# Kernel tuning notes

Measured on AMD Instinct MI355X. Metric: run time of the kernel, lower is better.

## Reference

```python
import jax, jax.numpy as jnp
import numpy as np

NUM_HEADS = 16
HEAD_DIM = 64  # hidden_size // num_heads


def _logsparse_allowed(seq_len):
    # allowed[i, j] True if key j is attended by query i:
    # j == i, j == i-1, or j == i - 2^k (k >= 1); combined with causal (j <= i).
    i = jnp.arange(seq_len)[:, None]
    j = jnp.arange(seq_len)[None, :]
    diff = i - j
    pow2 = (diff > 0) & ((diff & (diff - 1)) == 0)  # covers diff==1 and diff==2^k
    return (diff == 0) | pow2  # implies diff >= 0, so causal is subsumed


def setup_inputs() -> dict:
    key = jax.random.key(0)
    ks = jax.random.split(key, 7)
    B, S, H = 4, 2048, 1024
    return {
        "hidden_states": jax.random.normal(ks[0], (B, S, H), dtype=jnp.float32),
        "attention_mask": jnp.zeros((B, 1, 1, S), dtype=jnp.float32),
        "Wq": jax.random.normal(ks[1], (H, H), dtype=jnp.float32) * 0.02,
        "bq": jnp.zeros((H,), dtype=jnp.float32),
        "Wk": jax.random.normal(ks[2], (H, H), dtype=jnp.float32) * 0.02,
        "bk": jnp.zeros((H,), dtype=jnp.float32),
        "Wv": jax.random.normal(ks[3], (H, H), dtype=jnp.float32) * 0.02,
        "bv": jnp.zeros((H,), dtype=jnp.float32),
    }


def _split_heads(x):
    B, S, _ = x.shape
    return x.reshape(B, S, NUM_HEADS, HEAD_DIM).transpose(0, 2, 1, 3)  # b h t d


def reference(hidden_states, attention_mask, Wq, bq, Wk, bk, Wv, bv):
    B, S, H = hidden_states.shape
    q = _split_heads(hidden_states @ Wq.T + bq)
    k = _split_heads(hidden_states @ Wk.T + bk)
    v = _split_heads(hidden_states @ Wv.T + bv)

    scores = jnp.einsum("bhqd,bhkd->bhqk", q, k) * (HEAD_DIM ** -0.5)
    allowed = _logsparse_allowed(S)  # [S, S] bool
    scores = jnp.where(allowed[None, None], scores, -jnp.inf)
    scores = scores + attention_mask  # [B,1,1,S] additive mask
    probs = jax.nn.softmax(scores, axis=-1)
    out = jnp.einsum("bhqk,bhkd->bhqd", probs, v)
    return out.transpose(0, 2, 1, 3).reshape(B, S, H)
```

## Files before the change

### kernel.cpp

```cpp
#include <hip/hip_runtime.h>
#include <hip/hip_bf16.h>

#define S_LEN   2048
#define NHEADS  16
#define HDIM    64
#define HID     1024
#define BATCH   4
#define M_ROWS  (BATCH * S_LEN)

#define BM 128
#define BN 128
#define BK 32

typedef __attribute__((ext_vector_type(8))) short short8;
typedef __attribute__((ext_vector_type(4))) float floatx4;

__device__ __forceinline__ unsigned short f2bf_rne(float x) {
  union { float f; unsigned u; } v; v.f = x;
  unsigned r = v.u + 0x7fffu + ((v.u >> 16) & 1u);
  return (unsigned short)(r >> 16);
}

__device__ __forceinline__ float bf2f(unsigned short u) {
  union { unsigned u; float f; } c; c.u = ((unsigned)u) << 16;
  return c.f;
}

__device__ __forceinline__ void glds16(const unsigned short* g, unsigned short* l) {
  __builtin_amdgcn_global_load_lds(
      (const __attribute__((address_space(1))) unsigned int*)g,
      (__attribute__((address_space(3))) unsigned int*)l, 16, 0, 0);
}

#define HS4 (M_ROWS * HID / 4)
#define W4  (HID * HID / 4)
__global__ __launch_bounds__(256) void cast_all(
    const float* __restrict__ hs, const float* __restrict__ Wq,
    const float* __restrict__ Wk, const float* __restrict__ Wv,
    unsigned short* __restrict__ hsb, unsigned short* __restrict__ wqb,
    unsigned short* __restrict__ wkb, unsigned short* __restrict__ wvb) {
  int idx = blockIdx.x * 256 + threadIdx.x;
  const float* in;
  unsigned short* out;
  int off;
  if (idx < HS4) {
    in = hs; out = hsb; off = idx;
  } else {
    int r = idx - HS4;
    int seg = r >> 18;
    off = r & (W4 - 1);
    in  = (seg == 0) ? Wq  : (seg == 1) ? Wk  : Wv;
    out = (seg == 0) ? wqb : (seg == 1) ? wkb : wvb;
  }
  float4 v = ((const float4*)in)[off];
  ushort4 o;
  o.x = f2bf_rne(v.x);
  o.y = f2bf_rne(v.y);
  o.z = f2bf_rne(v.z);
  o.w = f2bf_rne(v.w);
  ((ushort4*)out)[off] = o;
}

__global__ __launch_bounds__(256) void qkv_gemm(
    const unsigned short* __restrict__ A,
    const unsigned short* __restrict__ W0, const unsigned short* __restrict__ W1,
    const unsigned short* __restrict__ W2,
    const float* __restrict__ b0, const float* __restrict__ b1,
    const float* __restrict__ b2,
    unsigned short* __restrict__ O0, unsigned short* __restrict__ O1,
    unsigned short* __restrict__ O2) {
  const int K = HID;
  const int N = HID;
  const int z = blockIdx.z;
  const unsigned short* __restrict__ W = (z == 0) ? W0 : (z == 1) ? W1 : W2;
  const float* __restrict__ bias = (z == 0) ? b0 : (z == 1) ? b1 : b2;
  unsigned short* __restrict__ O = (z == 0) ? O0 : (z == 1) ? O1 : O2;

  __shared__ __align__(16) unsigned short As[BM * BK];
  __shared__ __align__(16) unsigned short Bs[BN * BK];

  const int tid = threadIdx.x;
  const int w = tid >> 6;
  const int lane = tid & 63;
  const int m0 = blockIdx.x * BM;
  const int n0 = blockIdx.y * BN;

  const int c0 = w * 2, c1 = w * 2 + 1;
  const int scol = (lane & 3) * 8;
  const int r0 = c0 * 16 + (lane >> 2);
  const int r1 = c1 * 16 + (lane >> 2);

  const unsigned short* gA0 = A + (size_t)(m0 + r0) * K + scol;
  const unsigned short* gA1 = A + (size_t)(m0 + r1) * K + scol;
  const unsigned short* gB0 = W + (size_t)(n0 + r0) * K + scol;
  const unsigned short* gB1 = W + (size_t)(n0 + r1) * K + scol;
  unsigned short* lA0 = As + c0 * 512;
  unsigned short* lA1 = As + c1 * 512;
  unsigned short* lB0 = Bs + c0 * 512;
  unsigned short* lB1 = Bs + c1 * 512;

  const int lrow = lane & 15;
  const int qd = lane >> 4;
  const int arow = (w & 1) * 64 + lrow;
  const int brow = (w >> 1) * 64 + lrow;

  floatx4 acc[4][4] = {};

  for (int k0 = 0; k0 < K; k0 += BK) {
    glds16(gA0 + k0, lA0);
    glds16(gA1 + k0, lA1);
    glds16(gB0 + k0, lB0);
    glds16(gB1 + k0, lB1);
    __syncthreads();

    short8 af[4], bf[4];
    #pragma unroll
    for (int im = 0; im < 4; ++im)
      af[im] = *(const short8*)(As + (arow + im * 16) * BK + qd * 8);
    #pragma unroll
    for (int in = 0; in < 4; ++in)
      bf[in] = *(const short8*)(Bs + (brow + in * 16) * BK + qd * 8);

    #pragma unroll
    for (int im = 0; im < 4; ++im)
      #pragma unroll
      for (int in = 0; in < 4; ++in)
        acc[im][in] = __builtin_amdgcn_mfma_f32_16x16x32_bf16(af[im], bf[in], acc[im][in], 0, 0, 0);
    __syncthreads();
  }

  #pragma unroll
  for (int im = 0; im < 4; ++im) {
    #pragma unroll
    for (int in = 0; in < 4; ++in) {
      const int col = n0 + (w >> 1) * 64 + in * 16 + lrow;
      const float bb = bias[col];
      #pragma unroll
      for (int r = 0; r < 4; ++r) {
        const int row = m0 + (w & 1) * 64 + im * 16 + (qd << 2) + r;
        O[(size_t)row * N + col] = f2bf_rne(acc[im][in][r] + bb);
      }
    }
  }
}

__global__ __launch_bounds__(256) void logsparse_attn(
    const unsigned short* __restrict__ Q, const unsigned short* __restrict__ K,
    const unsigned short* __restrict__ V, const float* __restrict__ mask,
    float* __restrict__ out) {
  const int tid = threadIdx.x;
  const int l = tid & 7;
  const int qglob = blockIdx.x * 32 + (tid >> 3);

  const int i = qglob & (S_LEN - 1);
  const int h = (qglob >> 11) & (NHEADS - 1);
  const int b = qglob >> 15;

  const size_t base = (size_t)b * S_LEN * HID + h * HDIM + l * 8;

  float qf[8];
  {
    short8 q8 = *(const short8*)(Q + base + (size_t)i * HID);
    #pragma unroll
    for (int e = 0; e < 8; ++e) qf[e] = bf2f((unsigned short)q8[e]);
  }

  int js[12];
  js[0] = i;
  int nj = 1;
  for (int dlt = 1; dlt <= i; dlt <<= 1) js[nj++] = i - dlt;

  float s[12];
  #pragma unroll
  for (int t = 0; t < 12; ++t) {
    if (t < nj) {
      const int j = js[t];
      short8 k8 = *(const short8*)(K + base + (size_t)j * HID);
      float p = 0.f;
      #pragma unroll
      for (int e = 0; e < 8; ++e) p += qf[e] * bf2f((unsigned short)k8[e]);
      p += __shfl_xor(p, 1, 64);
      p += __shfl_xor(p, 2, 64);
      p += __shfl_xor(p, 4, 64);
      s[t] = p * 0.125f + mask[b * S_LEN + j];
    } else {
      s[t] = -1e30f;
    }
  }

  float mx = s[0];
  #pragma unroll
  for (int t = 1; t < 12; ++t) mx = fmaxf(mx, s[t]);
  float lsum = 0.f;
  #pragma unroll
  for (int t = 0; t < 12; ++t) { s[t] = __expf(s[t] - mx); lsum += s[t]; }
  const float inv = 1.f / lsum;

  float o[8] = {};
  #pragma unroll
  for (int t = 0; t < 12; ++t) {
    if (t < nj) {
      short8 v8 = *(const short8*)(V + base + (size_t)js[t] * HID);
      #pragma unroll
      for (int e = 0; e < 8; ++e) o[e] += s[t] * bf2f((unsigned short)v8[e]);
    }
  }

  float* op = out + base + (size_t)i * HID;
  float4 o0 = {o[0] * inv, o[1] * inv, o[2] * inv, o[3] * inv};
  float4 o1 = {o[4] * inv, o[5] * inv, o[6] * inv, o[7] * inv};
  *(float4*)(op) = o0;
  *(float4*)(op + 4) = o1;
}

extern "C" void kernel_launch(void* const* d_in, const int* in_sizes, int n_in,
                              void* d_out, int out_size, void* d_ws, size_t ws_size,
                              hipStream_t stream) {
  const float* hs   = (const float*)d_in[0];
  const float* mask = (const float*)d_in[1];
  const float* Wq   = (const float*)d_in[2];
  const float* bq   = (const float*)d_in[3];
  const float* Wk   = (const float*)d_in[4];
  const float* bk   = (const float*)d_in[5];
  const float* Wv   = (const float*)d_in[6];
  const float* bv   = (const float*)d_in[7];
  float* out = (float*)d_out;

  unsigned short* hsb = (unsigned short*)d_ws;
  unsigned short* wqb = hsb + (size_t)M_ROWS * HID;
  unsigned short* wkb = wqb + (size_t)HID * HID;
  unsigned short* wvb = wkb + (size_t)HID * HID;
  unsigned short* Qb = wvb + (size_t)HID * HID;
  unsigned short* Kb = Qb + (size_t)M_ROWS * HID;
  unsigned short* Vb = Kb + (size_t)M_ROWS * HID;

  {
    int quads = HS4 + 3 * W4;
    cast_all<<<quads / 256, 256, 0, stream>>>(hs, Wq, Wk, Wv, hsb, wqb, wkb, wvb);
  }

  {
    dim3 grid(M_ROWS / BM, HID / BN, 3);
    qkv_gemm<<<grid, 256, 0, stream>>>(hsb, wqb, wkb, wvb, bq, bk, bv, Qb, Kb, Vb);
  }

  {
    int blocks = (BATCH * NHEADS * S_LEN) / 32;
    logsparse_attn<<<blocks, 256, 0, stream>>>(Qb, Kb, Vb, mask, out);
  }
}
```

Baseline: 195.2 us.

## Double GEMM K-tile with XOR-swizzled LDS and batch attention gathers upfront

The QKV GEMM K-tile grows from 32 to 64, so each barrier pair covers two MFMA k-steps. The LDS layout gets an XOR swizzle on 16-byte chunks to avoid bank conflicts on fragment reads. The attention kernel now pads the index list and issues all 12 K, V and mask loads before any compute, exposing memory-level parallelism instead of serialising loads inside predicated loops. This costs more registers and some redundant loads for short rows.

```diff
diff --git a/kernel.cpp b/kernel.cpp
--- a/kernel.cpp
+++ b/kernel.cpp
@@ -10,7 +10,7 @@
 
 #define BM 128
 #define BN 128
-#define BK 32
+#define BK 64
 
 typedef __attribute__((ext_vector_type(8))) short short8;
 typedef __attribute__((ext_vector_type(4))) float floatx4;
@@ -85,47 +85,55 @@
   const int m0 = blockIdx.x * BM;
   const int n0 = blockIdx.y * BN;
 
-  const int c0 = w * 2, c1 = w * 2 + 1;
-  const int scol = (lane & 3) * 8;
-  const int r0 = c0 * 16 + (lane >> 2);
-  const int r1 = c1 * 16 + (lane >> 2);
-
-  const unsigned short* gA0 = A + (size_t)(m0 + r0) * K + scol;
-  const unsigned short* gA1 = A + (size_t)(m0 + r1) * K + scol;
-  const unsigned short* gB0 = W + (size_t)(n0 + r0) * K + scol;
-  const unsigned short* gB1 = W + (size_t)(n0 + r1) * K + scol;
-  unsigned short* lA0 = As + c0 * 512;
-  unsigned short* lA1 = As + c1 * 512;
-  unsigned short* lB0 = Bs + c0 * 512;
-  unsigned short* lB1 = Bs + c1 * 512;
+  const int lr = lane >> 3;
+  const int cc = (lane & 7) ^ lr;
+  const unsigned short* gA[4];
+  const unsigned short* gB[4];
+  unsigned short* lA[4];
+  unsigned short* lB[4];
+  #pragma unroll
+  for (int u = 0; u < 4; ++u) {
+    const int seg = w * 4 + u;
+    const int r = seg * 8 + lr;
+    gA[u] = A + (size_t)(m0 + r) * K + cc * 8;
+    gB[u] = W + (size_t)(n0 + r) * K + cc * 8;
+    lA[u] = As + seg * 512;
+    lB[u] = Bs + seg * 512;
+  }
 
   const int lrow = lane & 15;
   const int qd = lane >> 4;
+  const int sw = lrow & 7;
   const int arow = (w & 1) * 64 + lrow;
   const int brow = (w >> 1) * 64 + lrow;
 
   floatx4 acc[4][4] = {};
 
   for (int k0 = 0; k0 < K; k0 += BK) {
-    glds16(gA0 + k0, lA0);
-    glds16(gA1 + k0, lA1);
-    glds16(gB0 + k0, lB0);
-    glds16(gB1 + k0, lB1);
+    #pragma unroll
+    for (int u = 0; u < 4; ++u) {
+      glds16(gA[u] + k0, lA[u]);
+      glds16(gB[u] + k0, lB[u]);
+    }
     __syncthreads();
 
-    short8 af[4], bf[4];
-    #pragma unroll
-    for (int im = 0; im < 4; ++im)
-      af[im] = *(const short8*)(As + (arow + im * 16) * BK + qd * 8);
-    #pragma unroll
-    for (int in = 0; in < 4; ++in)
-      bf[in] = *(const short8*)(Bs + (brow + in * 16) * BK + qd * 8);
-
-    #pragma unroll
-    for (int im = 0; im < 4; ++im)
+    #pragma unroll
+    for (int kk = 0; kk < 2; ++kk) {
+      const int cp = (((kk << 2) | qd) ^ sw) * 8;
+      short8 af[4], bf[4];
+      #pragma unroll
+      for (int im = 0; im < 4; ++im)
+        af[im] = *(const short8*)(As + (arow + im * 16) * BK + cp);
       #pragma unroll
       for (int in = 0; in < 4; ++in)
-        acc[im][in] = __builtin_amdgcn_mfma_f32_16x16x32_bf16(af[im], bf[in], acc[im][in], 0, 0, 0);
+        bf[in] = *(const short8*)(Bs + (brow + in * 16) * BK + cp);
+
+      #pragma unroll
+      for (int im = 0; im < 4; ++im)
+        #pragma unroll
+        for (int in = 0; in < 4; ++in)
+          acc[im][in] = __builtin_amdgcn_mfma_f32_16x16x32_bf16(af[im], bf[in], acc[im][in], 0, 0, 0);
+    }
     __syncthreads();
   }
 
@@ -158,34 +166,41 @@
 
   const size_t base = (size_t)b * S_LEN * HID + h * HDIM + l * 8;
 
-  float qf[8];
-  {
-    short8 q8 = *(const short8*)(Q + base + (size_t)i * HID);
-    #pragma unroll
-    for (int e = 0; e < 8; ++e) qf[e] = bf2f((unsigned short)q8[e]);
-  }
-
   int js[12];
   js[0] = i;
   int nj = 1;
-  for (int dlt = 1; dlt <= i; dlt <<= 1) js[nj++] = i - dlt;
+  for (int d = 1; d <= i; d <<= 1) js[nj++] = i - d;
+  #pragma unroll
+  for (int t = 0; t < 12; ++t)
+    if (t >= nj) js[t] = i;
+
+  short8 k8[12], v8[12];
+  #pragma unroll
+  for (int t = 0; t < 12; ++t)
+    k8[t] = *(const short8*)(K + base + (size_t)js[t] * HID);
+  const short8 q8 = *(const short8*)(Q + base + (size_t)i * HID);
+  #pragma unroll
+  for (int t = 0; t < 12; ++t)
+    v8[t] = *(const short8*)(V + base + (size_t)js[t] * HID);
+  float mk[12];
+  #pragma unroll
+  for (int t = 0; t < 12; ++t)
+    mk[t] = mask[b * S_LEN + js[t]];
+
+  float qf[8];
+  #pragma unroll
+  for (int e = 0; e < 8; ++e) qf[e] = bf2f((unsigned short)q8[e]);
 
   float s[12];
   #pragma unroll
   for (int t = 0; t < 12; ++t) {
-    if (t < nj) {
-      const int j = js[t];
-      short8 k8 = *(const short8*)(K + base + (size_t)j * HID);
-      float p = 0.f;
-      #pragma unroll
-      for (int e = 0; e < 8; ++e) p += qf[e] * bf2f((unsigned short)k8[e]);
-      p += __shfl_xor(p, 1, 64);
-      p += __shfl_xor(p, 2, 64);
-      p += __shfl_xor(p, 4, 64);
-      s[t] = p * 0.125f + mask[b * S_LEN + j];
-    } else {
-      s[t] = -1e30f;
-    }
+    float p = 0.f;
+    #pragma unroll
+    for (int e = 0; e < 8; ++e) p += qf[e] * bf2f((unsigned short)k8[t][e]);
+    p += __shfl_xor(p, 1, 64);
+    p += __shfl_xor(p, 2, 64);
+    p += __shfl_xor(p, 4, 64);
+    s[t] = (t < nj) ? (p * 0.125f + mk[t]) : -1e30f;
   }
 
   float mx = s[0];
@@ -199,11 +214,8 @@
   float o[8] = {};
   #pragma unroll
   for (int t = 0; t < 12; ++t) {
-    if (t < nj) {
-      short8 v8 = *(const short8*)(V + base + (size_t)js[t] * HID);
-      #pragma unroll
-      for (int e = 0; e < 8; ++e) o[e] += s[t] * bf2f((unsigned short)v8[e]);
-    }
+    #pragma unroll
+    for (int e = 0; e < 8; ++e) o[e] += s[t] * bf2f((unsigned short)v8[t][e]);
   }
 
   float* op = out + base + (size_t)i * HID;
```

Measured after the change: 186.0 us. 4.7% less time.
